# Kernel optimization log

Hardware: AMD Instinct MI355X
Metric: run time of the kernel (lower is better)

Reference implementation:

```python
import jax, jax.numpy as jnp
import numpy as np

N_REFLNS = 4_194_304
N_DIM = 64
N_IMAGES = 1024


def setup_inputs() -> dict:
    key = jax.random.key(0)
    kx, kid = jax.random.split(key)
    x = jax.random.normal(kx, (N_REFLNS, N_DIM), dtype=jnp.float32)
    image_id = jnp.sort(jax.random.randint(kid, (N_REFLNS,), 0, N_IMAGES, dtype=jnp.int32))
    return {"x": x, "image_id": image_id, "n_images": N_IMAGES}


def reference(x, image_id, n_images):
    # torch.unique(return_inverse, return_counts) over ids 0..n_images-1 with all
    # ids present: unique ids == arange(n_images), inverse indices == image_id.
    counts = jax.ops.segment_sum(
        jnp.ones_like(image_id), image_id, num_segments=n_images
    )  # [n_images] int
    sums = jax.ops.segment_sum(x, image_id, num_segments=n_images)  # [n_images, n_dim]
    # guard against an (astronomically unlikely) empty segment
    denom = jnp.maximum(counts, 1).astype(x.dtype)[:, None]
    averaged = sums / denom
    return averaged, image_id, counts
```

## Files before the change

kernel.cpp:

```cpp
#include <hip/hip_runtime.h>

#define N_DIM          64
#define N_IMAGES       1024
#define ROWS_PER_BLOCK 2048
#define THREADS        256

typedef float v4f __attribute__((ext_vector_type(4)));
typedef int   v4i __attribute__((ext_vector_type(4)));

__device__ __forceinline__ v4f ldx(const float* __restrict__ p) {
    return __builtin_nontemporal_load((const v4f*)p);
}

__global__ __launch_bounds__(THREADS) void ImageAverage_phaseA(
    const float* __restrict__ x,
    const int*   __restrict__ ids,
    float*       __restrict__ accum,
    int*         __restrict__ counts,
    float*       __restrict__ out_id)
{
    const int t = threadIdx.x;
    const long long blockRow0 = (long long)blockIdx.x * ROWS_PER_BLOCK;

    {
        const v4i* idv  = (const v4i*)(ids + blockRow0);
        v4f*       outv = (v4f*)(out_id + blockRow0);
        const int niter = ROWS_PER_BLOCK / 4 / THREADS;
        #pragma unroll
        for (int k = 0; k < niter; ++k) {
            v4i v = idv[k * THREADS + t];
            v4f f;
            f.x = (float)v.x; f.y = (float)v.y; f.z = (float)v.z; f.w = (float)v.w;
            __builtin_nontemporal_store(f, &outv[k * THREADS + t]);
        }
    }

    const int dimGroup = t & 15;
    const int d0       = dimGroup * 4;
    const int rowOff   = t >> 4;
    const bool isCounter = (dimGroup == 0);

    v4f sum = {0.f, 0.f, 0.f, 0.f};
    int cnt = 0;

    long long row = blockRow0 + rowOff;
    int cur = ids[row];

    auto consume = [&](v4f a, v4f b, v4f c, v4f d, int idLast, long long grow) {
        if (idLast == cur) {
            sum += (a + b) + (c + d);
            cnt += 4;
        } else {
            #pragma unroll
            for (int k = 0; k < 4; ++k) {
                const int id = (k < 3) ? ids[grow + 16 * k] : idLast;
                const v4f v = (k == 0) ? a : (k == 1) ? b : (k == 2) ? c : d;
                if (id != cur) {
                    float* ap = accum + (long long)cur * N_DIM + d0;
                    atomicAdd(ap + 0, sum.x);
                    atomicAdd(ap + 1, sum.y);
                    atomicAdd(ap + 2, sum.z);
                    atomicAdd(ap + 3, sum.w);
                    if (isCounter) atomicAdd(&counts[cur], cnt);
                    sum = (v4f){0.f, 0.f, 0.f, 0.f};
                    cnt = 0;
                    cur = id;
                }
                sum += v;
                cnt++;
            }
        }
    };

    const int NGROUPS = ROWS_PER_BLOCK / 16 / 4;

    v4f a = ldx(x + row * N_DIM + d0);
    v4f b = ldx(x + (row + 16) * N_DIM + d0);
    v4f c = ldx(x + (row + 32) * N_DIM + d0);
    v4f d = ldx(x + (row + 48) * N_DIM + d0);
    int idLast = ids[row + 48];

    for (int g = 0; g < NGROUPS - 1; ++g) {
        const long long rown = row + 64;
        const v4f an = ldx(x + rown * N_DIM + d0);
        const v4f bn = ldx(x + (rown + 16) * N_DIM + d0);
        const v4f cn = ldx(x + (rown + 32) * N_DIM + d0);
        const v4f dn = ldx(x + (rown + 48) * N_DIM + d0);
        const int idLn = ids[rown + 48];

        consume(a, b, c, d, idLast, row);

        a = an; b = bn; c = cn; d = dn; idLast = idLn; row = rown;
    }

    consume(a, b, c, d, idLast, row);

    {
        float* ap = accum + (long long)cur * N_DIM + d0;
        atomicAdd(ap + 0, sum.x);
        atomicAdd(ap + 1, sum.y);
        atomicAdd(ap + 2, sum.z);
        atomicAdd(ap + 3, sum.w);
        if (isCounter) atomicAdd(&counts[cur], cnt);
    }
}

__global__ __launch_bounds__(THREADS) void ImageAverage_phaseB(
    const float* __restrict__ accum,
    const int*   __restrict__ counts,
    float*       __restrict__ out_avg,
    float*       __restrict__ out_counts)
{
    const int i = blockIdx.x * blockDim.x + threadIdx.x;
    if (i < N_IMAGES * N_DIM) {
        const int img = i >> 6;
        const int c = counts[img];
        const float denom = (float)(c > 0 ? c : 1);
        out_avg[i] = accum[i] / denom;
    }
    if (i < N_IMAGES) {
        out_counts[i] = (float)counts[i];
    }
}

extern "C" void kernel_launch(void* const* d_in, const int* in_sizes, int n_in,
                              void* d_out, int out_size, void* d_ws, size_t ws_size,
                              hipStream_t stream) {
    const float* x   = (const float*)d_in[0];
    const int*   ids = (const int*)d_in[1];
    const int n_reflns = in_sizes[1];

    float* out_avg    = (float*)d_out;
    float* out_id     = out_avg + (size_t)N_IMAGES * N_DIM;
    float* out_counts = out_id + (size_t)n_reflns;

    float* accum  = (float*)d_ws;
    int*   counts = (int*)((char*)d_ws + (size_t)N_IMAGES * N_DIM * sizeof(float));

    hipMemsetAsync(d_ws, 0,
                   (size_t)N_IMAGES * N_DIM * sizeof(float) + (size_t)N_IMAGES * sizeof(int),
                   stream);

    const int gridA = n_reflns / ROWS_PER_BLOCK;
    ImageAverage_phaseA<<<gridA, THREADS, 0, stream>>>(x, ids, accum, counts, out_id);

    const int nB = N_IMAGES * N_DIM;
    ImageAverage_phaseB<<<(nB + THREADS - 1) / THREADS, THREADS, 0, stream>>>(
        accum, counts, out_avg, out_counts);
}
```

Baseline: 1.339 ms.

## Deepen row prefetch to eight, drop nontemporal loads, accumulate directly into outputs

Each thread now prefetches eight rows per group instead of four, raising memory-level parallelism in the streaming segmented reduction. The nontemporal load hint on x is removed in favour of plain vector loads. Partial sums and counts are accumulated atomically straight into the output buffers, with counts kept as floats, so the workspace and the count conversion in the second kernel go away. This costs more registers per thread, which may lower occupancy, and adds a second memset launch.

```diff
diff --git a/kernel.cpp b/kernel.cpp
--- a/kernel.cpp
+++ b/kernel.cpp
@@ -4,19 +4,17 @@
 #define N_IMAGES       1024
 #define ROWS_PER_BLOCK 2048
 #define THREADS        256
+#define GROUP          8
+#define STRIDE         16
 
 typedef float v4f __attribute__((ext_vector_type(4)));
 typedef int   v4i __attribute__((ext_vector_type(4)));
 
-__device__ __forceinline__ v4f ldx(const float* __restrict__ p) {
-    return __builtin_nontemporal_load((const v4f*)p);
-}
-
 __global__ __launch_bounds__(THREADS) void ImageAverage_phaseA(
     const float* __restrict__ x,
     const int*   __restrict__ ids,
-    float*       __restrict__ accum,
-    int*         __restrict__ counts,
+    float*       __restrict__ out_avg,
+    float*       __restrict__ out_counts,
     float*       __restrict__ out_id)
 {
     const int t = threadIdx.x;
@@ -25,9 +23,8 @@
     {
         const v4i* idv  = (const v4i*)(ids + blockRow0);
         v4f*       outv = (v4f*)(out_id + blockRow0);
-        const int niter = ROWS_PER_BLOCK / 4 / THREADS;
         #pragma unroll
-        for (int k = 0; k < niter; ++k) {
+        for (int k = 0; k < ROWS_PER_BLOCK / 4 / THREADS; ++k) {
             v4i v = idv[k * THREADS + t];
             v4f f;
             f.x = (float)v.x; f.y = (float)v.y; f.z = (float)v.z; f.w = (float)v.w;
@@ -40,86 +37,82 @@
     const int rowOff   = t >> 4;
     const bool isCounter = (dimGroup == 0);
 
-    v4f sum = {0.f, 0.f, 0.f, 0.f};
-    int cnt = 0;
+    v4f  sum = {0.f, 0.f, 0.f, 0.f};
+    float cnt = 0.f;
 
     long long row = blockRow0 + rowOff;
     int cur = ids[row];
 
-    auto consume = [&](v4f a, v4f b, v4f c, v4f d, int idLast, long long grow) {
+    v4f va[GROUP], vb[GROUP];
+    int idA, idB;
+
+    auto consume = [&](const v4f (&v)[GROUP], int idLast, long long grow) {
         if (idLast == cur) {
-            sum += (a + b) + (c + d);
-            cnt += 4;
+            sum += ((v[0] + v[1]) + (v[2] + v[3])) + ((v[4] + v[5]) + (v[6] + v[7]));
+            cnt += (float)GROUP;
         } else {
             #pragma unroll
-            for (int k = 0; k < 4; ++k) {
-                const int id = (k < 3) ? ids[grow + 16 * k] : idLast;
-                const v4f v = (k == 0) ? a : (k == 1) ? b : (k == 2) ? c : d;
+            for (int k = 0; k < GROUP; ++k) {
+                const int id = (k < GROUP - 1) ? ids[grow + STRIDE * k] : idLast;
                 if (id != cur) {
-                    float* ap = accum + (long long)cur * N_DIM + d0;
+                    float* ap = out_avg + (long long)cur * N_DIM + d0;
                     atomicAdd(ap + 0, sum.x);
                     atomicAdd(ap + 1, sum.y);
                     atomicAdd(ap + 2, sum.z);
                     atomicAdd(ap + 3, sum.w);
-                    if (isCounter) atomicAdd(&counts[cur], cnt);
+                    if (isCounter) atomicAdd(&out_counts[cur], cnt);
                     sum = (v4f){0.f, 0.f, 0.f, 0.f};
-                    cnt = 0;
+                    cnt = 0.f;
                     cur = id;
                 }
-                sum += v;
-                cnt++;
+                sum += v[k];
+                cnt += 1.f;
             }
         }
     };
 
-    const int NGROUPS = ROWS_PER_BLOCK / 16 / 4;
+    const int NGROUPS = ROWS_PER_BLOCK / STRIDE / GROUP;
 
-    v4f a = ldx(x + row * N_DIM + d0);
-    v4f b = ldx(x + (row + 16) * N_DIM + d0);
-    v4f c = ldx(x + (row + 32) * N_DIM + d0);
-    v4f d = ldx(x + (row + 48) * N_DIM + d0);
-    int idLast = ids[row + 48];
+    #pragma unroll
+    for (int k = 0; k < GROUP; ++k)
+        va[k] = *(const v4f*)(x + (row + STRIDE * k) * N_DIM + d0);
+    idA = ids[row + STRIDE * (GROUP - 1)];
 
     for (int g = 0; g < NGROUPS - 1; ++g) {
-        const long long rown = row + 64;
-        const v4f an = ldx(x + rown * N_DIM + d0);
-        const v4f bn = ldx(x + (rown + 16) * N_DIM + d0);
-        const v4f cn = ldx(x + (rown + 32) * N_DIM + d0);
-        const v4f dn = ldx(x + (rown + 48) * N_DIM + d0);
-        const int idLn = ids[rown + 48];
+        const long long rowN = row + STRIDE * GROUP;
+        #pragma unroll
+        for (int k = 0; k < GROUP; ++k)
+            vb[k] = *(const v4f*)(x + (rowN + STRIDE * k) * N_DIM + d0);
+        idB = ids[rowN + STRIDE * (GROUP - 1)];
 
-        consume(a, b, c, d, idLast, row);
+        consume(va, idA, row);
 
-        a = an; b = bn; c = cn; d = dn; idLast = idLn; row = rown;
+        #pragma unroll
+        for (int k = 0; k < GROUP; ++k) va[k] = vb[k];
+        idA = idB;
+        row = rowN;
     }
-
-    consume(a, b, c, d, idLast, row);
+    consume(va, idA, row);
 
     {
-        float* ap = accum + (long long)cur * N_DIM + d0;
+        float* ap = out_avg + (long long)cur * N_DIM + d0;
         atomicAdd(ap + 0, sum.x);
         atomicAdd(ap + 1, sum.y);
         atomicAdd(ap + 2, sum.z);
         atomicAdd(ap + 3, sum.w);
-        if (isCounter) atomicAdd(&counts[cur], cnt);
+        if (isCounter) atomicAdd(&out_counts[cur], cnt);
     }
 }
 
 __global__ __launch_bounds__(THREADS) void ImageAverage_phaseB(
-    const float* __restrict__ accum,
-    const int*   __restrict__ counts,
     float*       __restrict__ out_avg,
-    float*       __restrict__ out_counts)
+    const float* __restrict__ out_counts)
 {
     const int i = blockIdx.x * blockDim.x + threadIdx.x;
     if (i < N_IMAGES * N_DIM) {
-        const int img = i >> 6;
-        const int c = counts[img];
-        const float denom = (float)(c > 0 ? c : 1);
-        out_avg[i] = accum[i] / denom;
-    }
-    if (i < N_IMAGES) {
-        out_counts[i] = (float)counts[i];
+        const float c = out_counts[i >> 6];
+        const float denom = (c > 0.f) ? c : 1.f;
+        out_avg[i] = out_avg[i] / denom;
     }
 }
 
@@ -134,17 +127,13 @@
     float* out_id     = out_avg + (size_t)N_IMAGES * N_DIM;
     float* out_counts = out_id + (size_t)n_reflns;
 
-    float* accum  = (float*)d_ws;
-    int*   counts = (int*)((char*)d_ws + (size_t)N_IMAGES * N_DIM * sizeof(float));
-
-    hipMemsetAsync(d_ws, 0,
-                   (size_t)N_IMAGES * N_DIM * sizeof(float) + (size_t)N_IMAGES * sizeof(int),
-                   stream);
+    hipMemsetAsync(out_avg,    0, (size_t)N_IMAGES * N_DIM * sizeof(float), stream);
+    hipMemsetAsync(out_counts, 0, (size_t)N_IMAGES * sizeof(float), stream);
 
     const int gridA = n_reflns / ROWS_PER_BLOCK;
-    ImageAverage_phaseA<<<gridA, THREADS, 0, stream>>>(x, ids, accum, counts, out_id);
+    ImageAverage_phaseA<<<gridA, THREADS, 0, stream>>>(x, ids, out_avg, out_counts, out_id);
 
     const int nB = N_IMAGES * N_DIM;
     ImageAverage_phaseB<<<(nB + THREADS - 1) / THREADS, THREADS, 0, stream>>>(
-        accum, counts, out_avg, out_counts);
+        out_avg, out_counts);
 }
```

New measurement: 1.367 ms. 2.0% more time.
